# Kernel optimization log

Hardware: AMD Instinct MI355X
Metric: run time of the kernel (lower is better)

The kernel has to match this reference:

```python
import jax, jax.numpy as jnp
import numpy as np

HEAD_SIZE = 64


def setup_inputs() -> dict:
    key = jax.random.key(0)
    ks = jax.random.split(key, 10)
    B, S, D, H, hs = 4, 2048, 768, 12, HEAD_SIZE
    F = 4 * D
    sd = lambda n: 1.0 / np.sqrt(n)
    return {
        "x": jax.random.normal(ks[0], (B, S, D), jnp.float32),
        "Wq": jax.random.normal(ks[1], (H, D, hs), jnp.float32) * sd(D),
        "Wk": jax.random.normal(ks[2], (H, D, hs), jnp.float32) * sd(D),
        "Wv": jax.random.normal(ks[3], (H, D, hs), jnp.float32) * sd(D),
        "Wo": jax.random.normal(ks[4], (D, D), jnp.float32) * sd(D),
        "bo": jnp.zeros((D,), jnp.float32),
        "W1": jax.random.normal(ks[5], (D, F), jnp.float32) * sd(D),
        "b1": jnp.zeros((F,), jnp.float32),
        "W2": jax.random.normal(ks[6], (F, D), jnp.float32) * sd(F),
        "b2": jnp.zeros((D,), jnp.float32),
    }


def reference(x, Wq, Wk, Wv, Wo, bo, W1, b1, W2, b2):
    B, S, D = x.shape
    hs = Wq.shape[-1]
    # per-head projections (no bias), vectorized over heads: [B,H,S,hs]
    q = jnp.einsum("bsd,hde->bhse", x, Wq)
    k = jnp.einsum("bsd,hde->bhse", x, Wk)
    v = jnp.einsum("bsd,hde->bhse", x, Wv)
    # causal attention scores [B,H,S,S], scaled by sqrt(head_size)
    scores = jnp.einsum("bhse,bhte->bhst", q, k) / jnp.sqrt(jnp.float32(hs))
    causal = jnp.tril(jnp.ones((S, S), dtype=bool))
    scores = jnp.where(causal, scores, -jnp.inf)
    attn = jax.nn.softmax(scores, axis=-1)
    z = jnp.einsum("bhst,bhte->bhse", attn, v)
    # concat heads along feature dim (head order preserved) -> [B,S,D]
    z = z.transpose(0, 2, 1, 3).reshape(B, S, D)
    # output projection + residual
    z = z @ Wo + bo + x
    # FFN + residual
    h = jax.nn.relu(z @ W1 + b1)
    return h @ W2 + b2 + z
```

## Files before the change

### kernel.cpp

```cpp
#include <hip/hip_runtime.h>


typedef __attribute__((ext_vector_type(4))) float f32x4;
typedef __attribute__((ext_vector_type(8))) short bf16x8;
typedef __attribute__((ext_vector_type(4))) unsigned short u16x4;

#define GLB_AS __attribute__((address_space(1)))
#define LDS_AS __attribute__((address_space(3)))

__device__ __forceinline__ unsigned short f2bf(float f) {
  unsigned int u = __float_as_uint(f);
  u = (u + 0x7FFFu + ((u >> 16) & 1u)) >> 16;
  return (unsigned short)u;
}

__device__ __forceinline__ void gload16(const void* g, void* l) {
  __builtin_amdgcn_global_load_lds((const GLB_AS unsigned int*)g,
                                   (LDS_AS unsigned int*)l, 16, 0, 0);
}

__device__ __forceinline__ int xcd_swz(int orig, int nwg) {
  int q = nwg >> 3, r = nwg & 7;
  int xcd = orig & 7, rest = orig >> 3;
  return (xcd < r ? xcd * (q + 1) : r * (q + 1) + (xcd - r) * q) + rest;
}

__global__ void castx(const float* __restrict__ in, unsigned short* __restrict__ out, int n) {
  int i = (blockIdx.x * 256 + threadIdx.x) * 4;
  if (i < n) {
    float4 f = *(const float4*)&in[i];
    u16x4 o;
    o[0] = f2bf(f.x); o[1] = f2bf(f.y); o[2] = f2bf(f.z); o[3] = f2bf(f.w);
    *(u16x4*)&out[i] = o;
  }
}

__global__ void tcast(const float* __restrict__ in, unsigned short* __restrict__ out,
                      int R, int C, float scale) {
  __shared__ float tile[32][33];
  const float* inb = in + (size_t)blockIdx.z * R * C;
  unsigned short* outb = out + (size_t)blockIdx.z * R * C;
  int bx = blockIdx.x * 32;
  int by = blockIdx.y * 32;
  int tx = threadIdx.x, ty = threadIdx.y;
  #pragma unroll
  for (int i = 0; i < 32; i += 8) {
    int r = by + ty + i, c = bx + tx;
    tile[ty + i][tx] = inb[(size_t)r * C + c];
  }
  __syncthreads();
  #pragma unroll
  for (int i = 0; i < 32; i += 8) {
    int c = bx + ty + i, r = by + tx;
    outb[(size_t)c * R + r] = f2bf(tile[tx][ty + i] * scale);
  }
}

__global__ void tcast3(const float* __restrict__ Wq, const float* __restrict__ Wk,
                       const float* __restrict__ Wv, unsigned short* __restrict__ out,
                       float qscale) {
  __shared__ float tile[32][33];
  const int R = 768, C = 64;
  int z = blockIdx.z, wsel = z / 12, head = z % 12;
  const float* in = (wsel == 0 ? Wq : wsel == 1 ? Wk : Wv) + (size_t)head * R * C;
  unsigned short* outb = out + (size_t)wsel * R * R + (size_t)head * R * C;
  float scale = wsel == 0 ? qscale : 1.0f;
  int bx = blockIdx.x * 32;
  int by = blockIdx.y * 32;
  int tx = threadIdx.x, ty = threadIdx.y;
  #pragma unroll
  for (int i = 0; i < 32; i += 8)
    tile[ty + i][tx] = in[(size_t)(by + ty + i) * C + bx + tx];
  __syncthreads();
  #pragma unroll
  for (int i = 0; i < 32; i += 8)
    outb[(size_t)(bx + ty + i) * R + by + tx] = f2bf(tile[tx][ty + i] * scale);
}

__global__ void vtrans(const unsigned short* __restrict__ v, unsigned short* __restrict__ vT) {
  __shared__ unsigned short tile[32][33];
  int bh = blockIdx.z, b = bh / 12, h = bh % 12;
  int s0 = blockIdx.x * 32, e0 = blockIdx.y * 32;
  int tx = threadIdx.x, ty = threadIdx.y;
  #pragma unroll
  for (int i = 0; i < 32; i += 8)
    tile[ty + i][tx] = v[(size_t)(b * 2048 + s0 + ty + i) * 768 + h * 64 + e0 + tx];
  __syncthreads();
  #pragma unroll
  for (int i = 0; i < 32; i += 8)
    vT[(size_t)((b * 12 + h) * 64 + e0 + ty + i) * 2048 + s0 + tx] = tile[tx][ty + i];
}

template <int EPI>
__global__ void gemm_bf16(const unsigned short* __restrict__ A,
                          const unsigned short* __restrict__ Bt,
                          const float* __restrict__ bias,
                          const float* __restrict__ resid,
                          float* __restrict__ Cf,
                          unsigned short* __restrict__ Cb,
                          int M, int N, int K, int gx, size_t segN) {
  __shared__ unsigned short Alds[128 * 32];
  __shared__ unsigned short Blds[128 * 32];
  const int tid = threadIdx.x;
  const int lane = tid & 63;
  const int w = tid >> 6;
  const int wm = w & 1, wn = w >> 1;
  const int wg = xcd_swz(blockIdx.x, gridDim.x);
  const int bm = (wg % gx) * 128, bn = (wg / gx) * 128;

  f32x4 acc[4][4] = {};

  const int r0 = tid >> 2;
  const int c0 = (tid & 3) * 8;

  for (int k0 = 0; k0 < K; k0 += 32) {
    __syncthreads();
    #pragma unroll
    for (int i = 0; i < 2; ++i) {
      int row = r0 + i * 64;
      gload16(&A[(size_t)(bm + row) * K + k0 + c0], &Alds[row * 32 + c0]);
      gload16(&Bt[(size_t)(bn + row) * K + k0 + c0], &Blds[row * 32 + c0]);
    }
    __syncthreads();
    bf16x8 af[4], bf[4];
    #pragma unroll
    for (int m = 0; m < 4; ++m)
      af[m] = *(const bf16x8*)&Alds[(wm * 64 + m * 16 + (lane & 15)) * 32 + (lane >> 4) * 8];
    #pragma unroll
    for (int n = 0; n < 4; ++n)
      bf[n] = *(const bf16x8*)&Blds[(wn * 64 + n * 16 + (lane & 15)) * 32 + (lane >> 4) * 8];
    #pragma unroll
    for (int m = 0; m < 4; ++m)
      #pragma unroll
      for (int n = 0; n < 4; ++n)
        acc[m][n] = __builtin_amdgcn_mfma_f32_16x16x32_bf16(af[m], bf[n], acc[m][n], 0, 0, 0);
  }

  const int crow0 = bm + wm * 64 + (lane >> 4) * 4;
  const int ccol0 = bn + wn * 64 + (lane & 15);
  const int seg = bn / 768;
  const int lcol0 = (bn % 768) + wn * 64 + (lane & 15);
  #pragma unroll
  for (int m = 0; m < 4; ++m) {
    #pragma unroll
    for (int n = 0; n < 4; ++n) {
      int col = ccol0 + n * 16;
      #pragma unroll
      for (int r = 0; r < 4; ++r) {
        int row = crow0 + m * 16 + r;
        float v = acc[m][n][r];
        if constexpr (EPI & 1) v += bias[col];
        if constexpr (EPI & 4) v += resid[(size_t)row * N + col];
        if constexpr (EPI & 2) v = fmaxf(v, 0.f);
        if constexpr (EPI & 8) Cf[(size_t)row * N + col] = v;
        if constexpr (EPI & 16) Cb[(size_t)row * N + col] = f2bf(v);
        if constexpr (EPI & 32)
          Cb[(size_t)seg * segN + (size_t)row * 768 + lcol0 + n * 16] = f2bf(v);
      }
    }
  }
}

__global__ void attn_fwd(const unsigned short* __restrict__ q,
                         const unsigned short* __restrict__ k,
                         const unsigned short* __restrict__ vT,
                         unsigned short* __restrict__ z) {
  __shared__ unsigned short Klds[2 * 2 * 64 * 32];
  __shared__ unsigned short Vlds[2 * 2 * 64 * 32];
  __shared__ unsigned short Plds[4 * 16 * 72];

  const int wgid = xcd_swz(blockIdx.x, gridDim.x);
  const int pi = wgid & 15;
  const int bh = wgid >> 4;
  const int b = bh / 12, h = bh % 12;
  const int tid = threadIdx.x, lane = tid & 63, w = tid >> 6;
  const int q16 = lane & 15;
  const int qt  = lane >> 4;
  const int rdc = ((qt ^ (lane & 3)) * 8);

  const int srow = tid >> 2;
  const int sdc  = (tid & 3) * 8;
  const int sgc  = (((tid & 3) ^ (srow & 3)) * 8);
  const size_t kbase = (size_t)(b * 2048) * 768 + h * 64;
  const size_t vbase = (size_t)((b * 12 + h) * 64) * 2048;
  unsigned short* Pw = &Plds[w * 16 * 72];

  #pragma unroll 1
  for (int seg = 0; seg < 2; ++seg) {
    const int qb = seg == 0 ? pi : 31 - pi;
    const int q0 = qb * 64;
    const int nt = qb + 1;

    const int qrow = q0 + w * 16 + q16;
    const size_t qoff = (size_t)(b * 2048 + qrow) * 768 + h * 64 + qt * 8;
    bf16x8 qf0 = *(const bf16x8*)&q[qoff];
    bf16x8 qf1 = *(const bf16x8*)&q[qoff + 32];

    f32x4 accO[4] = {};
    float mrow = -3.0e38f, lrow = 0.f;

    #pragma unroll
    for (int i = 0; i < 2; ++i) {
      gload16(&k[kbase + (size_t)srow * 768 + i * 32 + sgc],
              &Klds[i * 2048 + srow * 32 + sdc]);
      gload16(&vT[vbase + (size_t)srow * 2048 + i * 32 + sgc],
              &Vlds[i * 2048 + srow * 32 + sdc]);
    }
    __syncthreads();

    int buf = 0;
    for (int t = 0; t < nt; ++t) {
      if (t + 1 < nt) {
        const int kv1 = (t + 1) * 64;
        const int bo = (buf ^ 1) * 4096;
        #pragma unroll
        for (int i = 0; i < 2; ++i) {
          gload16(&k[kbase + (size_t)(kv1 + srow) * 768 + i * 32 + sgc],
                  &Klds[bo + i * 2048 + srow * 32 + sdc]);
          gload16(&vT[vbase + (size_t)srow * 2048 + kv1 + i * 32 + sgc],
                  &Vlds[bo + i * 2048 + srow * 32 + sdc]);
        }
      }

      const int kv0 = t * 64;
      const int kb_ = buf * 4096;

      f32x4 s[4];
      #pragma unroll
      for (int n = 0; n < 4; ++n) {
        bf16x8 kf0 = *(const bf16x8*)&Klds[kb_ + 0 * 2048 + (n * 16 + q16) * 32 + rdc];
        bf16x8 kf1 = *(const bf16x8*)&Klds[kb_ + 1 * 2048 + (n * 16 + q16) * 32 + rdc];
        f32x4 acc0 = {};
        acc0 = __builtin_amdgcn_mfma_f32_16x16x32_bf16(kf0, qf0, acc0, 0, 0, 0);
        s[n] = __builtin_amdgcn_mfma_f32_16x16x32_bf16(kf1, qf1, acc0, 0, 0, 0);
      }

      if (t == nt - 1) {
        const int rowg = q0 + w * 16 + q16;
        #pragma unroll
        for (int n = 0; n < 4; ++n)
          #pragma unroll
          for (int r = 0; r < 4; ++r)
            if (kv0 + n * 16 + qt * 4 + r > rowg) s[n][r] = -3.0e38f;
      }

      float pm = s[0][0];
      #pragma unroll
      for (int n = 0; n < 4; ++n)
        #pragma unroll
        for (int r = 0; r < 4; ++r) pm = fmaxf(pm, s[n][r]);
      pm = fmaxf(pm, __shfl_xor(pm, 16));
      pm = fmaxf(pm, __shfl_xor(pm, 32));

      if (__any(pm > mrow + 8.f)) {
        float mnew = fmaxf(mrow, pm);
        float sc = exp2f(mrow - mnew);
        mrow = mnew;
        lrow *= sc;
        int isc = __float_as_int(sc);
        #pragma unroll
        for (int r = 0; r < 4; ++r) {
          float scr = __int_as_float(__builtin_amdgcn_ds_bpermute((qt * 4 + r) * 4, isc));
          #pragma unroll
          for (int n = 0; n < 4; ++n) accO[n][r] *= scr;
        }
      }

      float psum = 0.f;
      #pragma unroll
      for (int n = 0; n < 4; ++n)
        #pragma unroll
        for (int r = 0; r < 4; ++r) { s[n][r] = exp2f(s[n][r] - mrow); psum += s[n][r]; }
      psum += __shfl_xor(psum, 16);
      psum += __shfl_xor(psum, 32);
      lrow += psum;

      #pragma unroll
      for (int n = 0; n < 4; ++n) {
        unsigned int lo, hi;
        asm("v_cvt_pk_bf16_f32 %0, %1, %2" : "=v"(lo) : "v"(s[n][0]), "v"(s[n][1]));
        asm("v_cvt_pk_bf16_f32 %0, %1, %2" : "=v"(hi) : "v"(s[n][2]), "v"(s[n][3]));
        uint2 pk; pk.x = lo; pk.y = hi;
        *(uint2*)&Pw[q16 * 72 + n * 16 + qt * 4] = pk;
      }

      #pragma unroll
      for (int kk = 0; kk < 2; ++kk) {
        bf16x8 pf = *(const bf16x8*)&Pw[q16 * 72 + kk * 32 + qt * 8];
        #pragma unroll
        for (int n = 0; n < 4; ++n) {
          bf16x8 vf = *(const bf16x8*)&Vlds[kb_ + kk * 2048 + (n * 16 + q16) * 32 + rdc];
          accO[n] = __builtin_amdgcn_mfma_f32_16x16x32_bf16(pf, vf, accO[n], 0, 0, 0);
        }
      }

      __syncthreads();
      buf ^= 1;
    }

    #pragma unroll
    for (int r = 0; r < 4; ++r) {
      float lr = __int_as_float(__builtin_amdgcn_ds_bpermute((qt * 4 + r) * 4,
                                                             __float_as_int(lrow)));
      float linv = 1.0f / lr;
      int rowg = q0 + w * 16 + qt * 4 + r;
      #pragma unroll
      for (int n = 0; n < 4; ++n)
        z[(size_t)(b * 2048 + rowg) * 768 + h * 64 + n * 16 + q16]
            = f2bf(accO[n][r] * linv);
    }
  }
}

extern "C" void kernel_launch(void* const* d_in, const int* in_sizes, int n_in,
                              void* d_out, int out_size, void* d_ws, size_t ws_size,
                              hipStream_t stream) {
  const float* x  = (const float*)d_in[0];
  const float* Wq = (const float*)d_in[1];
  const float* Wk = (const float*)d_in[2];
  const float* Wv = (const float*)d_in[3];
  const float* Wo = (const float*)d_in[4];
  const float* bo = (const float*)d_in[5];
  const float* W1 = (const float*)d_in[6];
  const float* b1 = (const float*)d_in[7];
  const float* W2 = (const float*)d_in[8];
  const float* b2 = (const float*)d_in[9];
  float* out = (float*)d_out;

  const int B = 4, S = 2048, D = 768, H = 12, hs = 64, F = 3072;
  const int M = B * S;
  const size_t MD = (size_t)M * D;

  unsigned short* xb   = (unsigned short*)d_ws;
  unsigned short* qb   = xb + MD;
  unsigned short* kb   = qb + MD;
  unsigned short* vb   = kb + MD;
  unsigned short* hbuf = xb;
  unsigned short* vT   = vb + MD;
  unsigned short* zb   = vT + MD;
  float*          z2f  = (float*)(zb + MD);
  unsigned short* z2b  = (unsigned short*)(z2f + MD);
  unsigned short* wqkvT= z2b + MD;
  unsigned short* woT  = wqkvT + 3 * (size_t)D * D;
  unsigned short* w1T  = woT + (size_t)D * D;
  unsigned short* w2T  = w1T + (size_t)D * F;

  dim3 tb(32, 8);

  castx<<<dim3((int)(MD / 4 / 256)), 256, 0, stream>>>(x, xb, (int)MD);

  const float QS = 0.125f * 1.4426950408889634f;
  tcast3<<<dim3(hs / 32, D / 32, 3 * H), tb, 0, stream>>>(Wq, Wk, Wv, wqkvT, QS);
  tcast<<<dim3(D / 32, D / 32, 1), tb, 0, stream>>>(Wo, woT, D, D, 1.0f);
  tcast<<<dim3(F / 32, D / 32, 1), tb, 0, stream>>>(W1, w1T, D, F, 1.0f);
  tcast<<<dim3(D / 32, F / 32, 1), tb, 0, stream>>>(W2, w2T, F, D, 1.0f);

  {
    int gx = M / 128, gy = 3 * D / 128;
    gemm_bf16<32><<<dim3(gx * gy), 256, 0, stream>>>(xb, wqkvT, nullptr, nullptr,
                                                     nullptr, qb, M, 3 * D, D, gx, MD);
  }

  vtrans<<<dim3(S / 32, hs / 32, B * H), tb, 0, stream>>>(vb, vT);

  attn_fwd<<<dim3((S / 128) * B * H), 256, 0, stream>>>(qb, kb, vT, zb);

  {
    int gx = M / 128, gy = D / 128;
    gemm_bf16<1 | 4 | 8 | 16><<<dim3(gx * gy), 256, 0, stream>>>(zb, woT, bo, x,
                                                                 z2f, z2b, M, D, D, gx, 0);
  }
  {
    int gx = M / 128, gy = F / 128;
    gemm_bf16<1 | 2 | 16><<<dim3(gx * gy), 256, 0, stream>>>(z2b, w1T, b1, nullptr,
                                                             nullptr, hbuf, M, F, D, gx, 0);
  }
  {
    int gx = M / 128, gy = D / 128;
    gemm_bf16<1 | 4 | 8><<<dim3(gx * gy), 256, 0, stream>>>(hbuf, w2T, b2, z2f,
                                                            out, nullptr, M, D, F, gx, 0);
  }
}
```

Baseline: 308.5 us.

## Double-buffer GEMM LDS tiles and group-swizzle block mapping for L2 reuse

The bf16 GEMM now uses two LDS buffers and prefetches the next K-slice with global_load_lds while MFMAs run on the current one, which cuts one barrier per iteration. Block indices are remapped into groups of 8 M-tiles sweeping across N, so neighbouring workgroups share A and B tiles in L2. This doubles LDS use per block, which may lower occupancy. It also hardcodes M/128 = 64 in the launch grid.

```diff
diff --git a/kernel.cpp b/kernel.cpp
--- a/kernel.cpp
+++ b/kernel.cpp
@@ -98,42 +98,57 @@
                           const float* __restrict__ resid,
                           float* __restrict__ Cf,
                           unsigned short* __restrict__ Cb,
-                          int M, int N, int K, int gx, size_t segN) {
-  __shared__ unsigned short Alds[128 * 32];
-  __shared__ unsigned short Blds[128 * 32];
+                          int M, int N, int K, int gy, size_t segN) {
+  __shared__ unsigned short Alds[2][128 * 32];
+  __shared__ unsigned short Blds[2][128 * 32];
   const int tid = threadIdx.x;
   const int lane = tid & 63;
   const int w = tid >> 6;
   const int wm = w & 1, wn = w >> 1;
   const int wg = xcd_swz(blockIdx.x, gridDim.x);
-  const int bm = (wg % gx) * 128, bn = (wg / gx) * 128;
+  const int gsz = 8 * gy;
+  const int group = wg / gsz;
+  const int rem = wg - group * gsz;
+  const int bm = (group * 8 + (rem & 7)) * 128;
+  const int bn = (rem >> 3) * 128;
 
   f32x4 acc[4][4] = {};
 
   const int r0 = tid >> 2;
   const int c0 = (tid & 3) * 8;
 
+  #pragma unroll
+  for (int i = 0; i < 2; ++i) {
+    int row = r0 + i * 64;
+    gload16(&A[(size_t)(bm + row) * K + c0], &Alds[0][row * 32 + c0]);
+    gload16(&Bt[(size_t)(bn + row) * K + c0], &Blds[0][row * 32 + c0]);
+  }
+  __syncthreads();
+
+  int buf = 0;
   for (int k0 = 0; k0 < K; k0 += 32) {
-    __syncthreads();
-    #pragma unroll
-    for (int i = 0; i < 2; ++i) {
-      int row = r0 + i * 64;
-      gload16(&A[(size_t)(bm + row) * K + k0 + c0], &Alds[row * 32 + c0]);
-      gload16(&Bt[(size_t)(bn + row) * K + k0 + c0], &Blds[row * 32 + c0]);
-    }
-    __syncthreads();
+    if (k0 + 32 < K) {
+      #pragma unroll
+      for (int i = 0; i < 2; ++i) {
+        int row = r0 + i * 64;
+        gload16(&A[(size_t)(bm + row) * K + k0 + 32 + c0], &Alds[buf ^ 1][row * 32 + c0]);
+        gload16(&Bt[(size_t)(bn + row) * K + k0 + 32 + c0], &Blds[buf ^ 1][row * 32 + c0]);
+      }
+    }
     bf16x8 af[4], bf[4];
     #pragma unroll
     for (int m = 0; m < 4; ++m)
-      af[m] = *(const bf16x8*)&Alds[(wm * 64 + m * 16 + (lane & 15)) * 32 + (lane >> 4) * 8];
+      af[m] = *(const bf16x8*)&Alds[buf][(wm * 64 + m * 16 + (lane & 15)) * 32 + (lane >> 4) * 8];
     #pragma unroll
     for (int n = 0; n < 4; ++n)
-      bf[n] = *(const bf16x8*)&Blds[(wn * 64 + n * 16 + (lane & 15)) * 32 + (lane >> 4) * 8];
+      bf[n] = *(const bf16x8*)&Blds[buf][(wn * 64 + n * 16 + (lane & 15)) * 32 + (lane >> 4) * 8];
     #pragma unroll
     for (int m = 0; m < 4; ++m)
       #pragma unroll
       for (int n = 0; n < 4; ++n)
         acc[m][n] = __builtin_amdgcn_mfma_f32_16x16x32_bf16(af[m], bf[n], acc[m][n], 0, 0, 0);
+    __syncthreads();
+    buf ^= 1;
   }
 
   const int crow0 = bm + wm * 64 + (lane >> 4) * 4;
@@ -356,9 +371,9 @@
   tcast<<<dim3(D / 32, F / 32, 1), tb, 0, stream>>>(W2, w2T, F, D, 1.0f);
 
   {
-    int gx = M / 128, gy = 3 * D / 128;
-    gemm_bf16<32><<<dim3(gx * gy), 256, 0, stream>>>(xb, wqkvT, nullptr, nullptr,
-                                                     nullptr, qb, M, 3 * D, D, gx, MD);
+    int gy = 3 * D / 128;
+    gemm_bf16<32><<<dim3(64 * gy), 256, 0, stream>>>(xb, wqkvT, nullptr, nullptr,
+                                                     nullptr, qb, M, 3 * D, D, gy, MD);
   }
 
   vtrans<<<dim3(S / 32, hs / 32, B * H), tb, 0, stream>>>(vb, vT);
@@ -366,18 +381,18 @@
   attn_fwd<<<dim3((S / 128) * B * H), 256, 0, stream>>>(qb, kb, vT, zb);
 
   {
-    int gx = M / 128, gy = D / 128;
-    gemm_bf16<1 | 4 | 8 | 16><<<dim3(gx * gy), 256, 0, stream>>>(zb, woT, bo, x,
-                                                                 z2f, z2b, M, D, D, gx, 0);
+    int gy = D / 128;
+    gemm_bf16<1 | 4 | 8 | 16><<<dim3(64 * gy), 256, 0, stream>>>(zb, woT, bo, x,
+                                                                 z2f, z2b, M, D, D, gy, 0);
   }
   {
-    int gx = M / 128, gy = F / 128;
-    gemm_bf16<1 | 2 | 16><<<dim3(gx * gy), 256, 0, stream>>>(z2b, w1T, b1, nullptr,
-                                                             nullptr, hbuf, M, F, D, gx, 0);
+    int gy = F / 128;
+    gemm_bf16<1 | 2 | 16><<<dim3(64 * gy), 256, 0, stream>>>(z2b, w1T, b1, nullptr,
+                                                             nullptr, hbuf, M, F, D, gy, 0);
   }
   {
-    int gx = M / 128, gy = D / 128;
-    gemm_bf16<1 | 4 | 8><<<dim3(gx * gy), 256, 0, stream>>>(hbuf, w2T, b2, z2f,
-                                                            out, nullptr, M, D, F, gx, 0);
-  }
-}
+    int gy = D / 128;
+    gemm_bf16<1 | 4 | 8><<<dim3(64 * gy), 256, 0, stream>>>(hbuf, w2T, b2, z2f,
+                                                            out, nullptr, M, D, F, gy, 0);
+  }
+}
```

Measured after the change: 288.6 us. 1.07x faster.
